# Performance work log

Measured on AMD Instinct MI355X. Metric: run time of the kernel, lower is better.

Reference implementation:

```python
import jax, jax.numpy as jnp
from jax import lax
import numpy as np

N_ATOMS, N_BONDS, N_GRAPHS = 8192, 32768, 256
EMBED, HIDDEN, DEPTH = 32, 256, 10
ATOM_VOCAB, BOND_VOCAB = 200, 10


def setup_inputs() -> dict:
    key = jax.random.key(0)
    ks = jax.random.split(key, 16)
    f = lambda k, *sh: jax.random.normal(k, sh, dtype=jnp.float32) * 0.05
    return {
        "atom_features": jax.random.randint(ks[0], (N_ATOMS,), 0, ATOM_VOCAB),
        "bond_features": jax.random.randint(ks[1], (N_BONDS,), 0, BOND_VOCAB),
        "adjacency_matrix": jax.random.randint(ks[2], (N_ATOMS, N_ATOMS), 0, 2, dtype=jnp.int32),
        "batch_indices": jax.random.randint(ks[3], (N_ATOMS,), 0, N_GRAPHS),
        "atom_emb": f(ks[4], ATOM_VOCAB, EMBED),
        "bond_emb": f(ks[5], BOND_VOCAB, EMBED),
        "msg_W": f(ks[6], DEPTH, HIDDEN, 2 * EMBED),
        "msg_b": f(ks[7], DEPTH, HIDDEN),
        "gru_Wih": f(ks[8], DEPTH, 3 * EMBED, HIDDEN),
        "gru_Whh": f(ks[9], DEPTH, 3 * EMBED, EMBED),
        "gru_bih": f(ks[10], DEPTH, 3 * EMBED),
        "gru_bhh": f(ks[11], DEPTH, 3 * EMBED),
        "pool_W": f(ks[12], HIDDEN, EMBED),
        "pool_b": f(ks[13], HIDDEN),
    }


def _gmpn(atom_emb, bond_emb, msg_W, msg_b, gru_Wih, gru_Whh, gru_bih, gru_bhh,
          pool_W, pool_b, atom_features, bond_features, adjacency_matrix, batch_indices):
    H = atom_emb[atom_features]                       # [N, E]
    A = (adjacency_matrix > 0).astype(H.dtype)        # [N, N] 0/1
    deg = A.sum(axis=1)                               # [N]
    has_nb = deg > 0
    inv_deg = jnp.where(has_nb, 1.0 / jnp.maximum(deg, 1.0), 0.0)[:, None]

    def layer(h, params):
        W, b, wih, whh, b_ih, b_hh = params
        # mean_j Linear([h_i ; h_j]) = W1 h_i + W2 mean_j h_j + b
        neigh_mean = (A @ h) * inv_deg                # [N, E]
        W1, W2 = W[:, :EMBED], W[:, EMBED:]
        msg = h @ W1.T + neigh_mean @ W2.T + b        # [N, HIDDEN]
        msg = jnp.where(has_nb[:, None], msg, 0.0)    # zero message if no neighbors
        # single-step GRU: input=msg, hidden state=h
        gi = msg @ wih.T + b_ih
        gh = h @ whh.T + b_hh
        ir, iz, inn = jnp.split(gi, 3, axis=-1)
        hr, hz, hn = jnp.split(gh, 3, axis=-1)
        r = jax.nn.sigmoid(ir + hr)
        z = jax.nn.sigmoid(iz + hz)
        n = jnp.tanh(inn + r * hn)
        h_new = (1.0 - z) * n + z * h                 # [N, E]
        return h_new, None

    H, _ = lax.scan(layer, H, (msg_W, msg_b, gru_Wih, gru_Whh, gru_bih, gru_bhh))

    # per-graph mean pooling (zeros for empty graphs), then global_pool linear
    seg_sum = jax.ops.segment_sum(H, batch_indices, num_segments=N_GRAPHS)
    cnt = jax.ops.segment_sum(jnp.ones((H.shape[0],), H.dtype), batch_indices, num_segments=N_GRAPHS)
    graph_mean = jnp.where(cnt[:, None] > 0, seg_sum / jnp.maximum(cnt, 1.0)[:, None], 0.0)
    graph_embeddings = graph_mean @ pool_W.T + pool_b  # [G, HIDDEN]

    bond_embeddings = bond_emb[bond_features]          # [B, E]
    return H, bond_embeddings, graph_embeddings


def reference(atom_features, bond_features, adjacency_matrix, batch_indices,
              atom_emb, bond_emb, msg_W, msg_b, gru_Wih, gru_Whh, gru_bih, gru_bhh,
              pool_W, pool_b):
    return _gmpn(atom_emb, bond_emb, msg_W, msg_b, gru_Wih, gru_Whh, gru_bih, gru_bhh,
                 pool_W, pool_b, atom_features, bond_features, adjacency_matrix, batch_indices)
```

## Files before the change

### kernel.cpp

```cpp
#include <hip/hip_runtime.h>
#include <stdint.h>

typedef __bf16 bf16x8 __attribute__((ext_vector_type(8)));
typedef float f32x4 __attribute__((ext_vector_type(4)));

__device__ __forceinline__ float b2f(unsigned short u){
  unsigned int t = ((unsigned int)u) << 16;
  return __builtin_bit_cast(float, t);
}
__device__ __forceinline__ unsigned short f2b(float f){
  unsigned int x = __builtin_bit_cast(unsigned int, f);
  x = x + 0x7FFFu + ((x >> 16) & 1u);
  return (unsigned short)(x >> 16);
}
__device__ __forceinline__ void spread8(unsigned int B, unsigned int w[4]){
  unsigned int m = __umul24(B, 0x8001u);
  w[0] = __umul24(m & 0x00010001u, 0x3F80u);
  w[1] = __umul24(m & 0x00040004u, 0x0FE0u);
  w[2] = __umul24(m & 0x00100010u, 0x03F8u);
  w[3] = __umul24(m & 0x00400040u, 0x00FEu);
}
__device__ __forceinline__ float fsig(float x){ return 1.f/(1.f + __expf(-x)); }
__device__ __forceinline__ float ftanh(float x){ return 1.f - 2.f/(__expf(2.f*x) + 1.f); }

__global__ void k_prep(const void* s_msgW, const void* s_msgb, const void* s_wih,
                       const void* s_whh, const void* s_bih, const void* s_bhh,
                       const void* s_poolW, const void* s_poolb,
                       const unsigned short* __restrict__ aemb_u16,
                       unsigned short* __restrict__ cw,
                       int* __restrict__ deg, float* __restrict__ seg,
                       float* __restrict__ cnt, int* __restrict__ flag){
  int b = blockIdx.x, t = threadIdx.x;
  unsigned int uu = aemb_u16[2*t];
  int e = (int)((uu >> 7) & 0xFF);
  unsigned long long vote = __ballot(e >= 100 && e <= 127);
  int isb = (__popcll(vote) > 32) ? 1 : 0;
  if (b < 1771){
    int id = b*256 + t;
    if (id < 453248){
      const void* src; int off;
      if      (id < 163840){ src = s_msgW;  off = id; }
      else if (id < 166400){ src = s_msgb;  off = id - 163840; }
      else if (id < 412160){ src = s_wih;   off = id - 166400; }
      else if (id < 442880){ src = s_whh;   off = id - 412160; }
      else if (id < 443840){ src = s_bih;   off = id - 442880; }
      else if (id < 444800){ src = s_bhh;   off = id - 443840; }
      else if (id < 452992){ src = s_poolW; off = id - 444800; }
      else                 { src = s_poolb; off = id - 452992; }
      cw[id] = isb ? ((const unsigned short*)src)[off]
                   : f2b(((const float*)src)[off]);
    }
  } else {
    int id2 = (b - 1771)*256 + t;
    if (id2 < 8192){ deg[id2] = 0; seg[id2] = 0.f; }
    if (id2 < 256) cnt[id2] = 0.f;
    if (b == 1771 && t == 0) flag[0] = isb;
  }
}

__global__ void k_pack(const int* __restrict__ adj, unsigned int* __restrict__ mask3,
                       int* __restrict__ deg){
  int tid = blockIdx.x*256 + threadIdx.x;
  int rb  = tid >> 12;
  int rem = tid & 4095;
  int kgg = rem >> 6;
  int L   = rem & 63;
  int lc = L & 15, q = L >> 4;
  int row = rb*16 + lc;
  const int* arow = adj + (size_t)row*8192 + kgg*128 + q*8;
  unsigned int dw = 0; int pc = 0;
  #pragma unroll
  for (int s=0;s<4;s++){
    const int* p = arow + s*32;
    unsigned int b = 0;
    #pragma unroll
    for (int t=0;t<8;t++) b |= (p[t] > 0 ? 1u : 0u) << t;
    dw |= b << (8*s);
    pc += __popc(b);
  }
  mask3[tid] = dw;
  pc += __shfl_xor(pc, 16);
  pc += __shfl_xor(pc, 32);
  if (q == 0) atomicAdd(deg + row, pc);
}

__global__ void k_bond(const int* __restrict__ bft, const void* __restrict__ braw,
                       const int* __restrict__ flag,
                       unsigned short* __restrict__ outB16, float* __restrict__ outB32){
  int id = blockIdx.x*256 + threadIdx.x;
  int e = id >> 5, c = id & 31;
  int idx = bft[e]*32 + c;
  if (flag[0]) outB16[id] = ((const unsigned short*)braw)[idx];
  else         outB32[id] = ((const float*)braw)[idx];
}

__global__ void k_embed(const int* __restrict__ af, const void* __restrict__ araw,
                        const int* __restrict__ flag,
                        float* __restrict__ hf32, uint4* __restrict__ hfrag){
  __shared__ __align__(16) float sh[512];
  int t = threadIdx.x;
  int r = t >> 5, c = t & 31;
  int row = blockIdx.x*16 + r;
  int idx = af[row]*32 + c;
  float f;
  if (flag[0]) f = b2f(((const unsigned short*)araw)[idx]);
  else         f = ((const float*)araw)[idx];
  hf32[row*32 + c] = f;
  sh[r*32 + c] = f;
  __syncthreads();
  if (t < 64){
    int nt = t >> 5, Lq = t & 31;
    int ks32 = blockIdx.x >> 1, half = blockIdx.x & 1;
    int col = nt*16 + (Lq & 15);
    int rbase = (Lq >> 4)*8;
    unsigned int w[4];
    #pragma unroll
    for (int p=0;p<4;p++){
      unsigned int lo = f2b(sh[(rbase + 2*p    )*32 + col]);
      unsigned int hi = f2b(sh[(rbase + 2*p + 1)*32 + col]);
      w[p] = lo | (hi << 16);
    }
    hfrag[(ks32*2 + nt)*64 + half*32 + Lq] = make_uint4(w[0],w[1],w[2],w[3]);
  }
}

__launch_bounds__(512)
__global__ void k_layer(const unsigned int* __restrict__ mask3,
                        const uint4* __restrict__ hfragIn,
                        unsigned int* __restrict__ hfragOut,
                        float* __restrict__ hf32,
                        const int* __restrict__ deg,
                        const unsigned short* __restrict__ msgW,
                        const unsigned short* __restrict__ msgb,
                        const unsigned short* __restrict__ wih,
                        const unsigned short* __restrict__ whh,
                        const unsigned short* __restrict__ bih,
                        const unsigned short* __restrict__ bhh,
                        const int* __restrict__ bidx,
                        float* __restrict__ seg, float* __restrict__ cnt,
                        unsigned short* __restrict__ out16, float* __restrict__ out32,
                        const int* __restrict__ flag, int last)
{
  __shared__ __align__(16) char uni[33792];
  __shared__ __align__(16) unsigned short sA[32][72];
  __shared__ __align__(16) unsigned short smsg[32][264];
  __shared__ int sdeg[32];

  const int t = threadIdx.x;
  const int b = blockIdx.x;
  const int w = t >> 6, L = t & 63;
  const int q = L >> 4, lc = L & 15;
  const int rowbase = b*32;

  const int r0 = t >> 4;
  const int cl = t & 15;
  const int r  = rowbase + r0;
  const int isb = flag[0];
  const int dgr = deg[r];
  const float invr = dgr > 0 ? 1.f/(float)dgr : 0.f;
  float h0 = hf32[r*32 + cl];
  float h1 = hf32[r*32 + 16 + cl];
  sA[r0][cl]    = f2b(h0);
  sA[r0][16+cl] = f2b(h1);
  if (cl == 0) sdeg[r0] = dgr;

  {
    f32x4 a00={0,0,0,0}, a01={0,0,0,0}, a10={0,0,0,0}, a11={0,0,0,0};
    const unsigned int* mp = mask3 + (size_t)b*8192 + w*512 + L;
    const uint4* bp = hfragIn + (size_t)w*4096 + L;
    for (int g=0; g<8; g++){
      unsigned int mw0 = mp[g*64];
      unsigned int mw1 = mp[4096 + g*64];
      #pragma unroll
      for (int s=0; s<4; s++){
        int ks = g*4 + s;
        uint4 u0 = bp[ks*128];
        uint4 u1 = bp[ks*128 + 64];
        union { unsigned int u[4]; bf16x8 v; } A0, A1, B0, B1;
        spread8((mw0 >> (8*s)) & 0xFFu, A0.u);
        spread8((mw1 >> (8*s)) & 0xFFu, A1.u);
        B0.u[0]=u0.x; B0.u[1]=u0.y; B0.u[2]=u0.z; B0.u[3]=u0.w;
        B1.u[0]=u1.x; B1.u[1]=u1.y; B1.u[2]=u1.z; B1.u[3]=u1.w;
        a00 = __builtin_amdgcn_mfma_f32_16x16x32_bf16(A0.v, B0.v, a00, 0,0,0);
        a01 = __builtin_amdgcn_mfma_f32_16x16x32_bf16(A0.v, B1.v, a01, 0,0,0);
        a10 = __builtin_amdgcn_mfma_f32_16x16x32_bf16(A1.v, B0.v, a10, 0,0,0);
        a11 = __builtin_amdgcn_mfma_f32_16x16x32_bf16(A1.v, B1.v, a11, 0,0,0);
      }
    }
    float* sp = (float*)uni + w*1056;
    #pragma unroll
    for (int rg=0; rg<4; rg++){
      int rw = q*4 + rg;
      sp[rw*33 + lc]         = a00[rg];
      sp[rw*33 + 16 + lc]    = a01[rg];
      sp[(16+rw)*33 + lc]    = a10[rg];
      sp[(16+rw)*33 + 16+lc] = a11[rg];
    }
  }
  __syncthreads();
  {
    const float* spf = (const float*)uni;
    float s0 = 0.f, s1 = 0.f;
    #pragma unroll
    for (int ww=0; ww<8; ww++){
      s0 += spf[ww*1056 + r0*33 + cl];
      s1 += spf[ww*1056 + r0*33 + 16 + cl];
    }
    sA[r0][32+cl] = f2b(s0*invr);
    sA[r0][48+cl] = f2b(s1*invr);
  }
  __syncthreads();
  {
    int rt = w & 1, ntb = (w >> 1)*4;
    union { uint4 u; bf16x8 v; } A0, A1;
    A0.u = *(const uint4*)&sA[rt*16 + lc][q*8];
    A1.u = *(const uint4*)&sA[rt*16 + lc][32 + q*8];
    #pragma unroll
    for (int i=0; i<4; i++){
      int nt = ntb + i;
      union { uint4 u; bf16x8 v; } B0, B1;
      B0.u = *(const uint4*)(msgW + (size_t)(nt*16 + lc)*64 + q*8);
      B1.u = *(const uint4*)(msgW + (size_t)(nt*16 + lc)*64 + 32 + q*8);
      f32x4 am = {0,0,0,0};
      am = __builtin_amdgcn_mfma_f32_16x16x32_bf16(A0.v, B0.v, am, 0,0,0);
      am = __builtin_amdgcn_mfma_f32_16x16x32_bf16(A1.v, B1.v, am, 0,0,0);
      float bv = b2f(msgb[nt*16 + lc]);
      #pragma unroll
      for (int rg=0; rg<4; rg++){
        int rw = rt*16 + q*4 + rg;
        float v = am[rg] + bv;
        if (sdeg[rw] == 0) v = 0.f;
        smsg[rw][nt*16 + lc] = f2b(v);
      }
    }
  }
  __syncthreads();
  {
    float* sgi = (float*)uni;
    float* sgh = (float*)(uni + 12800);
    if (w < 6){
      int nt = w;
      f32x4 g0 = {0,0,0,0}, g1 = {0,0,0,0};
      #pragma unroll
      for (int ks=0; ks<8; ks++){
        union { uint4 u; bf16x8 v; } A0, A1, B;
        B.u  = *(const uint4*)(wih + (size_t)(nt*16 + lc)*256 + ks*32 + q*8);
        A0.u = *(const uint4*)&smsg[lc][ks*32 + q*8];
        A1.u = *(const uint4*)&smsg[16 + lc][ks*32 + q*8];
        g0 = __builtin_amdgcn_mfma_f32_16x16x32_bf16(A0.v, B.v, g0, 0,0,0);
        g1 = __builtin_amdgcn_mfma_f32_16x16x32_bf16(A1.v, B.v, g1, 0,0,0);
      }
      #pragma unroll
      for (int rg=0; rg<4; rg++){
        sgi[(q*4+rg)*100      + nt*16 + lc] = g0[rg];
        sgi[(16+q*4+rg)*100   + nt*16 + lc] = g1[rg];
      }
    } else {
      int rt = w - 6;
      union { uint4 u; bf16x8 v; } A;
      A.u = *(const uint4*)&sA[rt*16 + lc][q*8];
      #pragma unroll
      for (int nt=0; nt<6; nt++){
        union { uint4 u; bf16x8 v; } B;
        B.u = *(const uint4*)(whh + (size_t)(nt*16 + lc)*32 + q*8);
        f32x4 hh = {0,0,0,0};
        hh = __builtin_amdgcn_mfma_f32_16x16x32_bf16(A.v, B.v, hh, 0,0,0);
        #pragma unroll
        for (int rg=0; rg<4; rg++)
          sgh[(rt*16 + q*4+rg)*100 + nt*16 + lc] = hh[rg];
      }
    }
  }
  __syncthreads();
  {
    const float* sgi = (const float*)uni;
    const float* sgh = (const float*)(uni + 12800);
    float ir0 = sgi[r0*100 + cl]    + b2f(bih[cl]),    hr0 = sgh[r0*100 + cl]    + b2f(bhh[cl]);
    float iz0 = sgi[r0*100 + 32+cl] + b2f(bih[32+cl]), hz0 = sgh[r0*100 + 32+cl] + b2f(bhh[32+cl]);
    float in0 = sgi[r0*100 + 64+cl] + b2f(bih[64+cl]), hn0 = sgh[r0*100 + 64+cl] + b2f(bhh[64+cl]);
    float ir1 = sgi[r0*100 + 16+cl] + b2f(bih[16+cl]), hr1 = sgh[r0*100 + 16+cl] + b2f(bhh[16+cl]);
    float iz1 = sgi[r0*100 + 48+cl] + b2f(bih[48+cl]), hz1 = sgh[r0*100 + 48+cl] + b2f(bhh[48+cl]);
    float in1 = sgi[r0*100 + 80+cl] + b2f(bih[80+cl]), hn1 = sgh[r0*100 + 80+cl] + b2f(bhh[80+cl]);
    float rr0 = fsig(ir0 + hr0), zz0 = fsig(iz0 + hz0);
    float rr1 = fsig(ir1 + hr1), zz1 = fsig(iz1 + hz1);
    float nn0 = ftanh(in0 + rr0*hn0);
    float nn1 = ftanh(in1 + rr1*hn1);
    h0 = (1.f - zz0)*nn0 + zz0*h0;
    h1 = (1.f - zz1)*nn1 + zz1*h1;
    hf32[r*32 + cl]      = h0;
    hf32[r*32 + 16 + cl] = h1;
    unsigned int m0 = f2b(h0), m1 = f2b(h1);
    unsigned int p0 = (unsigned int)__shfl_xor((int)m0, 16);
    unsigned int p1 = (unsigned int)__shfl_xor((int)m1, 16);
    if ((r & 1) == 0){
      int ks32 = r >> 5;
      int Lf = ((r >> 3) & 3)*16 + cl;
      int pidx = (r & 7) >> 1;
      hfragOut[((ks32*2 + 0)*64 + Lf)*4 + pidx] = m0 | (p0 << 16);
      hfragOut[((ks32*2 + 1)*64 + Lf)*4 + pidx] = m1 | (p1 << 16);
    }
    if (last){
      if (isb){ out16[r*32 + cl] = (unsigned short)m0; out16[r*32 + 16 + cl] = (unsigned short)m1; }
      else    { out32[r*32 + cl] = h0; out32[r*32 + 16 + cl] = h1; }
      int gb = bidx[r];
      atomicAdd(seg + gb*32 + cl, h0);
      atomicAdd(seg + gb*32 + 16 + cl, h1);
      if (cl == 0) atomicAdd(cnt + gb, 1.f);
    }
  }
}

__global__ void k_pool(const float* __restrict__ seg, const float* __restrict__ cnt,
                       const unsigned short* __restrict__ pw, const unsigned short* __restrict__ pb,
                       const int* __restrict__ flag,
                       unsigned short* __restrict__ outG16, float* __restrict__ outG32){
  int g = blockIdx.x, o = threadIdx.x;
  float cv = cnt[g];
  float ic = cv > 0.f ? 1.f/cv : 0.f;
  float s = 0.f;
  #pragma unroll
  for (int c=0;c<32;c++) s += seg[g*32+c]*ic*b2f(pw[o*32+c]);
  s += b2f(pb[o]);
  if (flag[0]) outG16[g*256 + o] = f2b(s);
  else         outG32[g*256 + o] = s;
}

extern "C" void kernel_launch(void* const* d_in, const int* in_sizes, int n_in,
                              void* d_out, int out_size, void* d_ws, size_t ws_size,
                              hipStream_t stream){
  const int* af   = (const int*)d_in[0];
  const int* bft  = (const int*)d_in[1];
  const int* adj  = (const int*)d_in[2];
  const int* bidx = (const int*)d_in[3];

  char* ws = (char*)d_ws;
  unsigned int*   mask3  = (unsigned int*)(ws + 0);
  unsigned int*   hfrag0 = (unsigned int*)(ws + 8388608);
  unsigned int*   hfrag1 = (unsigned int*)(ws + 8912896);
  float*          hf32   = (float*)(ws + 9437184);
  int*            deg    = (int*)(ws + 10485760);
  float*          seg    = (float*)(ws + 10518528);
  float*          cnt    = (float*)(ws + 10551296);
  int*            flag   = (int*)(ws + 10552320);
  unsigned short* cw     = (unsigned short*)(ws + 10552384);

  unsigned short* o16 = (unsigned short*)d_out;
  float*          o32 = (float*)d_out;

  k_prep<<<1803, 256, 0, stream>>>(d_in[6], d_in[7], d_in[8], d_in[9], d_in[10],
                                   d_in[11], d_in[12], d_in[13],
                                   (const unsigned short*)d_in[4],
                                   cw, deg, seg, cnt, flag);
  k_pack<<<8192, 256, 0, stream>>>(adj, mask3, deg);
  k_bond<<<4096, 256, 0, stream>>>(bft, d_in[5], flag, o16 + 262144, o32 + 262144);
  k_embed<<<512, 512, 0, stream>>>(af, d_in[4], flag, hf32, (uint4*)hfrag0);

  for (int d = 0; d < 10; d++){
    const uint4*  hin  = (const uint4*)((d & 1) ? hfrag1 : hfrag0);
    unsigned int* hout = (d & 1) ? hfrag0 : hfrag1;
    k_layer<<<256, 512, 0, stream>>>(mask3, hin, hout, hf32, deg,
                                     cw + (size_t)d*16384,        cw + 163840 + d*256,
                                     cw + 166400 + (size_t)d*24576, cw + 412160 + d*3072,
                                     cw + 442880 + d*96,          cw + 443840 + d*96,
                                     bidx, seg, cnt, o16, o32, flag, (d == 9) ? 1 : 0);
  }
  k_pool<<<256, 256, 0, stream>>>(seg, cnt, cw + 444800, cw + 452992, flag,
                                  o16 + 1310720, o32 + 1310720);
}
```

Baseline: 532.7 us.

## Fuse init kernels and software-pipeline mask/feature loads in layer kernel

Merges the weight-conversion, adjacency packing and bond-embedding kernels into one launch, with a tiny separate kernel zeroing the degree array beforehand. In the layer kernel's aggregation loop, the next group's mask words and h fragments are prefetched into registers while the current group's MFMAs run, and it sets launch bounds to one block per SM. It also caches the per-row degree values in registers. This cuts launch overhead and hides global-load latency, at the cost of higher register pressure.

After: 533.4 us. No clear change (+0.1%).

```diff
diff --git a/kernel.cpp b/kernel.cpp
--- a/kernel.cpp
+++ b/kernel.cpp
@@ -23,20 +23,49 @@
 __device__ __forceinline__ float fsig(float x){ return 1.f/(1.f + __expf(-x)); }
 __device__ __forceinline__ float ftanh(float x){ return 1.f - 2.f/(__expf(2.f*x) + 1.f); }
 
-__global__ void k_prep(const void* s_msgW, const void* s_msgb, const void* s_wih,
+__global__ void k_init(const int* __restrict__ adj, unsigned int* __restrict__ mask3,
+                       int* __restrict__ deg,
+                       const void* s_msgW, const void* s_msgb, const void* s_wih,
                        const void* s_whh, const void* s_bih, const void* s_bhh,
                        const void* s_poolW, const void* s_poolb,
                        const unsigned short* __restrict__ aemb_u16,
+                       const int* __restrict__ bft, const void* __restrict__ braw,
                        unsigned short* __restrict__ cw,
-                       int* __restrict__ deg, float* __restrict__ seg,
-                       float* __restrict__ cnt, int* __restrict__ flag){
+                       float* __restrict__ seg, float* __restrict__ cnt,
+                       int* __restrict__ flag,
+                       unsigned short* __restrict__ outB16, float* __restrict__ outB32){
   int b = blockIdx.x, t = threadIdx.x;
+  if (b < 8192){
+    int tid = b*256 + t;
+    int rb  = tid >> 12;
+    int rem = tid & 4095;
+    int kgg = rem >> 6;
+    int L   = rem & 63;
+    int lc = L & 15, q = L >> 4;
+    int row = rb*16 + lc;
+    const int* arow = adj + (size_t)row*8192 + kgg*128 + q*8;
+    unsigned int dw = 0; int pc = 0;
+    #pragma unroll
+    for (int s=0;s<4;s++){
+      const int* p = arow + s*32;
+      unsigned int bb = 0;
+      #pragma unroll
+      for (int j=0;j<8;j++) bb |= (p[j] > 0 ? 1u : 0u) << j;
+      dw |= bb << (8*s);
+      pc += __popc(bb);
+    }
+    mask3[tid] = dw;
+    pc += __shfl_xor(pc, 16);
+    pc += __shfl_xor(pc, 32);
+    if (q == 0) atomicAdd(deg + row, pc);
+    return;
+  }
   unsigned int uu = aemb_u16[2*t];
   int e = (int)((uu >> 7) & 0xFF);
   unsigned long long vote = __ballot(e >= 100 && e <= 127);
   int isb = (__popcll(vote) > 32) ? 1 : 0;
-  if (b < 1771){
-    int id = b*256 + t;
+  if (b < 9963){
+    int id = (b - 8192)*256 + t;
     if (id < 453248){
       const void* src; int off;
       if      (id < 163840){ src = s_msgW;  off = id; }
@@ -50,48 +79,22 @@
       cw[id] = isb ? ((const unsigned short*)src)[off]
                    : f2b(((const float*)src)[off]);
     }
+  } else if (b < 9996){
+    int id2 = (b - 9963)*256 + t;
+    if (id2 < 8192) seg[id2] = 0.f;
+    if (id2 < 256) cnt[id2] = 0.f;
+    if (b == 9963 && t == 0) flag[0] = isb;
   } else {
-    int id2 = (b - 1771)*256 + t;
-    if (id2 < 8192){ deg[id2] = 0; seg[id2] = 0.f; }
-    if (id2 < 256) cnt[id2] = 0.f;
-    if (b == 1771 && t == 0) flag[0] = isb;
-  }
-}
-
-__global__ void k_pack(const int* __restrict__ adj, unsigned int* __restrict__ mask3,
-                       int* __restrict__ deg){
-  int tid = blockIdx.x*256 + threadIdx.x;
-  int rb  = tid >> 12;
-  int rem = tid & 4095;
-  int kgg = rem >> 6;
-  int L   = rem & 63;
-  int lc = L & 15, q = L >> 4;
-  int row = rb*16 + lc;
-  const int* arow = adj + (size_t)row*8192 + kgg*128 + q*8;
-  unsigned int dw = 0; int pc = 0;
-  #pragma unroll
-  for (int s=0;s<4;s++){
-    const int* p = arow + s*32;
-    unsigned int b = 0;
-    #pragma unroll
-    for (int t=0;t<8;t++) b |= (p[t] > 0 ? 1u : 0u) << t;
-    dw |= b << (8*s);
-    pc += __popc(b);
-  }
-  mask3[tid] = dw;
-  pc += __shfl_xor(pc, 16);
-  pc += __shfl_xor(pc, 32);
-  if (q == 0) atomicAdd(deg + row, pc);
-}
-
-__global__ void k_bond(const int* __restrict__ bft, const void* __restrict__ braw,
-                       const int* __restrict__ flag,
-                       unsigned short* __restrict__ outB16, float* __restrict__ outB32){
-  int id = blockIdx.x*256 + threadIdx.x;
-  int e = id >> 5, c = id & 31;
-  int idx = bft[e]*32 + c;
-  if (flag[0]) outB16[id] = ((const unsigned short*)braw)[idx];
-  else         outB32[id] = ((const float*)braw)[idx];
+    int id = (b - 9996)*256 + t;
+    int e2 = id >> 5, c = id & 31;
+    int idx = bft[e2]*32 + c;
+    if (isb) outB16[id] = ((const unsigned short*)braw)[idx];
+    else     outB32[id] = ((const float*)braw)[idx];
+  }
+}
+
+__global__ void k_zero(int* __restrict__ deg){
+  deg[blockIdx.x*256 + threadIdx.x] = 0;
 }
 
 __global__ void k_embed(const int* __restrict__ af, const void* __restrict__ araw,
@@ -124,7 +127,7 @@
   }
 }
 
-__launch_bounds__(512)
+__launch_bounds__(512, 1)
 __global__ void k_layer(const unsigned int* __restrict__ mask3,
                         const uint4* __restrict__ hfragIn,
                         unsigned int* __restrict__ hfragOut,
@@ -141,20 +144,17 @@
                         unsigned short* __restrict__ out16, float* __restrict__ out32,
                         const int* __restrict__ flag, int last)
 {
-  __shared__ __align__(16) char uni[33792];
+  __shared__ __align__(16) float uni[8448];
   __shared__ __align__(16) unsigned short sA[32][72];
   __shared__ __align__(16) unsigned short smsg[32][264];
   __shared__ int sdeg[32];
 
-  const int t = threadIdx.x;
-  const int b = blockIdx.x;
+  const int t = threadIdx.x, b = blockIdx.x;
   const int w = t >> 6, L = t & 63;
   const int q = L >> 4, lc = L & 15;
-  const int rowbase = b*32;
-
   const int r0 = t >> 4;
   const int cl = t & 15;
-  const int r  = rowbase + r0;
+  const int r  = b*32 + r0;
   const int isb = flag[0];
   const int dgr = deg[r];
   const float invr = dgr > 0 ? 1.f/(float)dgr : 0.f;
@@ -168,17 +168,29 @@
     f32x4 a00={0,0,0,0}, a01={0,0,0,0}, a10={0,0,0,0}, a11={0,0,0,0};
     const unsigned int* mp = mask3 + (size_t)b*8192 + w*512 + L;
     const uint4* bp = hfragIn + (size_t)w*4096 + L;
+    unsigned int mw0 = mp[0];
+    unsigned int mw1 = mp[4096];
+    uint4 cb[8];
+    #pragma unroll
+    for (int s=0;s<4;s++){ cb[2*s] = bp[s*128]; cb[2*s+1] = bp[s*128 + 64]; }
     for (int g=0; g<8; g++){
-      unsigned int mw0 = mp[g*64];
-      unsigned int mw1 = mp[4096 + g*64];
+      unsigned int nm0 = 0, nm1 = 0;
+      uint4 nb[8];
+      if (g < 7){
+        nm0 = mp[(g+1)*64];
+        nm1 = mp[4096 + (g+1)*64];
+        #pragma unroll
+        for (int s=0;s<4;s++){
+          nb[2*s]   = bp[((g+1)*4 + s)*128];
+          nb[2*s+1] = bp[((g+1)*4 + s)*128 + 64];
+        }
+      }
       #pragma unroll
       for (int s=0; s<4; s++){
-        int ks = g*4 + s;
-        uint4 u0 = bp[ks*128];
-        uint4 u1 = bp[ks*128 + 64];
         union { unsigned int u[4]; bf16x8 v; } A0, A1, B0, B1;
         spread8((mw0 >> (8*s)) & 0xFFu, A0.u);
         spread8((mw1 >> (8*s)) & 0xFFu, A1.u);
+        uint4 u0 = cb[2*s], u1 = cb[2*s+1];
         B0.u[0]=u0.x; B0.u[1]=u0.y; B0.u[2]=u0.z; B0.u[3]=u0.w;
         B1.u[0]=u1.x; B1.u[1]=u1.y; B1.u[2]=u1.z; B1.u[3]=u1.w;
         a00 = __builtin_amdgcn_mfma_f32_16x16x32_bf16(A0.v, B0.v, a00, 0,0,0);
@@ -186,8 +198,13 @@
         a10 = __builtin_amdgcn_mfma_f32_16x16x32_bf16(A1.v, B0.v, a10, 0,0,0);
         a11 = __builtin_amdgcn_mfma_f32_16x16x32_bf16(A1.v, B1.v, a11, 0,0,0);
       }
-    }
-    float* sp = (float*)uni + w*1056;
+      mw0 = nm0; mw1 = nm1;
+      if (g < 7){
+        #pragma unroll
+        for (int u=0;u<8;u++) cb[u] = nb[u];
+      }
+    }
+    float* sp = uni + w*1056;
     #pragma unroll
     for (int rg=0; rg<4; rg++){
       int rw = q*4 + rg;
@@ -199,12 +216,11 @@
   }
   __syncthreads();
   {
-    const float* spf = (const float*)uni;
     float s0 = 0.f, s1 = 0.f;
     #pragma unroll
     for (int ww=0; ww<8; ww++){
-      s0 += spf[ww*1056 + r0*33 + cl];
-      s1 += spf[ww*1056 + r0*33 + 16 + cl];
+      s0 += uni[ww*1056 + r0*33 + cl];
+      s1 += uni[ww*1056 + r0*33 + 16 + cl];
     }
     sA[r0][32+cl] = f2b(s0*invr);
     sA[r0][48+cl] = f2b(s1*invr);
@@ -215,6 +231,9 @@
     union { uint4 u; bf16x8 v; } A0, A1;
     A0.u = *(const uint4*)&sA[rt*16 + lc][q*8];
     A1.u = *(const uint4*)&sA[rt*16 + lc][32 + q*8];
+    int sd[4];
+    #pragma unroll
+    for (int rg=0; rg<4; rg++) sd[rg] = sdeg[rt*16 + q*4 + rg];
     #pragma unroll
     for (int i=0; i<4; i++){
       int nt = ntb + i;
@@ -229,15 +248,15 @@
       for (int rg=0; rg<4; rg++){
         int rw = rt*16 + q*4 + rg;
         float v = am[rg] + bv;
-        if (sdeg[rw] == 0) v = 0.f;
+        if (sd[rg] == 0) v = 0.f;
         smsg[rw][nt*16 + lc] = f2b(v);
       }
     }
   }
   __syncthreads();
   {
-    float* sgi = (float*)uni;
-    float* sgh = (float*)(uni + 12800);
+    float* sgi = uni;
+    float* sgh = uni + 3200;
     if (w < 6){
       int nt = w;
       f32x4 g0 = {0,0,0,0}, g1 = {0,0,0,0};
@@ -252,8 +271,8 @@
       }
       #pragma unroll
       for (int rg=0; rg<4; rg++){
-        sgi[(q*4+rg)*100      + nt*16 + lc] = g0[rg];
-        sgi[(16+q*4+rg)*100   + nt*16 + lc] = g1[rg];
+        sgi[(q*4+rg)*100    + nt*16 + lc] = g0[rg];
+        sgi[(16+q*4+rg)*100 + nt*16 + lc] = g1[rg];
       }
     } else {
       int rt = w - 6;
@@ -273,8 +292,8 @@
   }
   __syncthreads();
   {
-    const float* sgi = (const float*)uni;
-    const float* sgh = (const float*)(uni + 12800);
+    const float* sgi = uni;
+    const float* sgh = uni + 3200;
     float ir0 = sgi[r0*100 + cl]    + b2f(bih[cl]),    hr0 = sgh[r0*100 + cl]    + b2f(bhh[cl]);
     float iz0 = sgi[r0*100 + 32+cl] + b2f(bih[32+cl]), hz0 = sgh[r0*100 + 32+cl] + b2f(bhh[32+cl]);
     float in0 = sgi[r0*100 + 64+cl] + b2f(bih[64+cl]), hn0 = sgh[r0*100 + 64+cl] + b2f(bhh[64+cl]);
@@ -293,9 +312,7 @@
     unsigned int p0 = (unsigned int)__shfl_xor((int)m0, 16);
     unsigned int p1 = (unsigned int)__shfl_xor((int)m1, 16);
     if ((r & 1) == 0){
-      int ks32 = r >> 5;
-      int Lf = ((r >> 3) & 3)*16 + cl;
-      int pidx = (r & 7) >> 1;
+      int ks32 = r >> 5, Lf = ((r >> 3) & 3)*16 + cl, pidx = (r & 7) >> 1;
       hfragOut[((ks32*2 + 0)*64 + Lf)*4 + pidx] = m0 | (p0 << 16);
       hfragOut[((ks32*2 + 1)*64 + Lf)*4 + pidx] = m1 | (p1 << 16);
     }
@@ -347,21 +364,23 @@
   unsigned short* o16 = (unsigned short*)d_out;
   float*          o32 = (float*)d_out;
 
-  k_prep<<<1803, 256, 0, stream>>>(d_in[6], d_in[7], d_in[8], d_in[9], d_in[10],
-                                   d_in[11], d_in[12], d_in[13],
-                                   (const unsigned short*)d_in[4],
-                                   cw, deg, seg, cnt, flag);
-  k_pack<<<8192, 256, 0, stream>>>(adj, mask3, deg);
-  k_bond<<<4096, 256, 0, stream>>>(bft, d_in[5], flag, o16 + 262144, o32 + 262144);
+  k_zero<<<32, 256, 0, stream>>>(deg);
+  k_init<<<14092, 256, 0, stream>>>(adj, mask3, deg,
+                                    d_in[6], d_in[7], d_in[8], d_in[9], d_in[10],
+                                    d_in[11], d_in[12], d_in[13],
+                                    (const unsigned short*)d_in[4],
+                                    bft, d_in[5],
+                                    cw, seg, cnt, flag,
+                                    o16 + 262144, o32 + 262144);
   k_embed<<<512, 512, 0, stream>>>(af, d_in[4], flag, hf32, (uint4*)hfrag0);
 
   for (int d = 0; d < 10; d++){
     const uint4*  hin  = (const uint4*)((d & 1) ? hfrag1 : hfrag0);
     unsigned int* hout = (d & 1) ? hfrag0 : hfrag1;
     k_layer<<<256, 512, 0, stream>>>(mask3, hin, hout, hf32, deg,
-                                     cw + (size_t)d*16384,        cw + 163840 + d*256,
+                                     cw + (size_t)d*16384,          cw + 163840 + d*256,
                                      cw + 166400 + (size_t)d*24576, cw + 412160 + d*3072,
-                                     cw + 442880 + d*96,          cw + 443840 + d*96,
+                                     cw + 442880 + d*96,            cw + 443840 + d*96,
                                      bidx, seg, cnt, o16, o32, flag, (d == 9) ? 1 : 0);
   }
   k_pool<<<256, 256, 0, stream>>>(seg, cnt, cw + 444800, cw + 452992, flag,
```
